# Kernel optimization log

Measured on AMD Instinct MI355X. Metric: run time of the kernel, lower is better.

The kernel has to match this reference:

```python
import jax, jax.numpy as jnp
import numpy as np

N = 100000
E = 3200000
HID = 256
C = 10
T = 12
D = 8
HEADS = 4
LH = HID // 2  # LSTM hidden = hidden_dim // 2


def setup_inputs() -> dict:
    key = jax.random.key(0)
    ks = jax.random.split(key, 16)
    rn = lambda k, shp, s=0.05: jax.random.normal(k, shp, dtype=jnp.float32) * s
    return {
        "embeddings": jax.random.normal(ks[0], (N, HID), dtype=jnp.float32),
        "predictions": jax.random.normal(ks[1], (N, C), dtype=jnp.float32),
        "temporal_features": jax.random.normal(ks[2], (N, T, D), dtype=jnp.float32),
        "edge_index": jax.random.randint(ks[3], (2, E), 0, N),
        "cW1": rn(ks[4], (HID // 2, HID)), "cb1": jnp.zeros((HID // 2,), jnp.float32),
        "cW2": rn(ks[5], (1, HID // 2)), "cb2": jnp.zeros((1,), jnp.float32),
        "w_ih0": rn(ks[6], (4 * LH, C)), "w_hh0": rn(ks[7], (4 * LH, LH)),
        "b_ih0": jnp.zeros((4 * LH,), jnp.float32), "b_hh0": jnp.zeros((4 * LH,), jnp.float32),
        "w_ih1": rn(ks[8], (4 * LH, LH)), "w_hh1": rn(ks[9], (4 * LH, LH)),
        "b_ih1": jnp.zeros((4 * LH,), jnp.float32), "b_hh1": jnp.zeros((4 * LH,), jnp.float32),
        "gW": rn(ks[10], (C, HEADS * C)), "ga_src": rn(ks[11], (HEADS, C)),
        "ga_dst": rn(ks[12], (HEADS, C)), "gb": jnp.zeros((C,), jnp.float32),
    }


def _lstm_layer(x, w_ih, w_hh, b_ih, b_hh):
    # x: [N, T, I]; PyTorch gate order i, f, g, o
    n = x.shape[0]
    h_dim = w_hh.shape[1]
    def step(carry, xt):
        h, c = carry
        g = xt @ w_ih.T + h @ w_hh.T + b_ih + b_hh  # [N, 4H]
        i, f, gg, o = jnp.split(g, 4, axis=-1)
        c = jax.nn.sigmoid(f) * c + jax.nn.sigmoid(i) * jnp.tanh(gg)
        h = jax.nn.sigmoid(o) * jnp.tanh(c)
        return (h, c), h
    init = (jnp.zeros((n, h_dim), x.dtype), jnp.zeros((n, h_dim), x.dtype))
    _, hs = jax.lax.scan(step, init, jnp.swapaxes(x, 0, 1))  # [T, N, H]
    return jnp.swapaxes(hs, 0, 1)


def _gat(probs, src, dst, gW, ga_src, ga_dst, gb, n):
    x = (probs @ gW).reshape(n, HEADS, C)  # [N, H, C]
    a_s = (x * ga_src).sum(-1)  # [N, H]
    a_d = (x * ga_dst).sum(-1)
    e = jax.nn.leaky_relu(a_s[src] + a_d[dst], 0.2)  # [E, H]
    m = jax.ops.segment_max(e, dst, num_segments=n)
    ex = jnp.exp(e - m[dst])
    s = jax.ops.segment_sum(ex, dst, num_segments=n)
    alpha = ex / (s[dst] + 1e-16)  # edge softmax per destination
    out = jax.ops.segment_sum(alpha[:, :, None] * x[src], dst, num_segments=n)
    return out.mean(axis=1) + gb  # concat=False -> head mean, plus bias


def reference(embeddings, predictions, temporal_features, edge_index,
              cW1, cb1, cW2, cb2,
              w_ih0, w_hh0, b_ih0, b_hh0, w_ih1, w_hh1, b_ih1, b_hh1,
              gW, ga_src, ga_dst, gb):
    n = predictions.shape[0]
    probs = jax.nn.softmax(predictions, axis=-1)
    max_probs = probs.max(axis=-1)
    pseudo_labels = jnp.argmax(probs, axis=-1)

    # confidence_net (dropout inactive in eval)
    h = jax.nn.relu(embeddings @ cW1.T + cb1)
    embedding_confidence = jax.nn.sigmoid(h @ cW2.T + cb2)[:, 0]

    # temporal consistency: same prediction repeated T times through 2-layer LSTM
    t = temporal_features.shape[1]
    pred_seq = jnp.broadcast_to(predictions[:, None, :], (n, t, predictions.shape[1]))
    l1 = _lstm_layer(pred_seq, w_ih0, w_hh0, b_ih0, b_hh0)
    l2 = _lstm_layer(l1, w_ih1, w_hh1, b_ih1, b_hh1)
    temporal_variance = jnp.var(l2, axis=1, ddof=1).mean(axis=-1)  # torch.var unbiased
    temporal_confidence = 1.0 / (1.0 + temporal_variance)

    # self-loops (used by both GATConv and agreement check)
    loops = jnp.arange(n, dtype=edge_index.dtype)
    src = jnp.concatenate([edge_index[0], loops])
    dst = jnp.concatenate([edge_index[1], loops])

    gout = _gat(probs, src, dst, gW, ga_src, ga_dst, gb, n)
    num = (probs * gout).sum(-1)
    den = jnp.maximum(jnp.linalg.norm(probs, axis=-1) * jnp.linalg.norm(gout, axis=-1), 1e-8)
    graph_confidence = ((num / den) + 1.0) / 2.0

    combined = (0.4 * max_probs + 0.2 * embedding_confidence
                + 0.2 * temporal_confidence + 0.2 * graph_confidence)
    confident_mask = combined > 0.85

    # neighborhood agreement via segment-sum scatter (replaces per-edge loop)
    deg = jax.ops.segment_sum(jnp.ones_like(src, jnp.float32), src, num_segments=n)
    oh = jax.nn.one_hot(pseudo_labels, C, dtype=jnp.float32)
    nsum = jax.ops.segment_sum(oh[src], dst, num_segments=n)
    navg = nsum / (deg[:, None] + 1e-8)
    agreement = jnp.take_along_axis(navg, pseudo_labels[:, None], axis=1)[:, 0] >= 0.6
    final_mask = confident_mask & agreement

    entropy = -(probs * jnp.log(probs + 1e-8)).sum(-1)
    uncertainty = entropy / np.log(C).astype(np.float32)

    return (pseudo_labels, combined, final_mask, max_probs,
            embedding_confidence, temporal_confidence, graph_confidence, uncertainty)
```

## Files before the change

### kernel.cpp

```cpp
#include <hip/hip_runtime.h>
#include <hip/hip_bf16.h>


#define HIDN 256
#define NC 10
#define TSTEPS 12
#define NHEADS 4
#define LH 128

typedef __attribute__((ext_vector_type(8))) short short8;
typedef __attribute__((ext_vector_type(4))) float floatx4;

__device__ __forceinline__ unsigned short f2bf(float x) {
  unsigned u = __float_as_uint(x);
  u = u + 0x7FFFu + ((u >> 16) & 1u);
  return (unsigned short)(u >> 16);
}
__device__ __forceinline__ unsigned char f2fp8(float x) {
  return (unsigned char)(__builtin_amdgcn_cvt_pk_fp8_f32(x, 0.f, 0, false) & 0xff);
}
__device__ __forceinline__ float fexp2(float x) { return __builtin_amdgcn_exp2f(x); }
__device__ __forceinline__ float frcpf(float x) { return __builtin_amdgcn_rcpf(x); }
#define LOG2E 1.44269504f
__device__ __forceinline__ float sigf(float x) {
  return frcpf(1.0f + fexp2(-LOG2E * x));
}
__device__ __forceinline__ float sig2(float x) {
  return frcpf(1.f + fexp2(-LOG2E * x));
}
__device__ __forceinline__ float tanh2(float x) {
  return 1.f - 2.f * frcpf(1.f + fexp2((2.f * LOG2E) * x));
}
__device__ __forceinline__ floatx4 mfma16(short8 a, short8 b, floatx4 c) {
  return __builtin_amdgcn_mfma_f32_16x16x32_bf16(a, b, c, 0, 0, 0);
}
__device__ __forceinline__ floatx4 mfma8(long a, long b, floatx4 c) {
  return __builtin_amdgcn_mfma_f32_16x16x32_fp8_fp8(a, b, c, 0, 0, 0);
}

__device__ __forceinline__ void probs_body(
    int bb, float* sgW, float* sgas, float* sgad,
    const float* __restrict__ pred, const float* __restrict__ gW,
    const float* __restrict__ gas, const float* __restrict__ gad,
    float* __restrict__ out, float* __restrict__ wp12,
    float* __restrict__ was, float* __restrict__ wad,
    int* __restrict__ wlab, float* __restrict__ wmp, int N) {
  int tid = threadIdx.x;
  for (int i = tid; i < 400; i += 256) sgW[i] = gW[i];
  if (tid < 40) { sgas[tid] = gas[tid]; sgad[tid] = gad[tid]; }
  __syncthreads();
  int node = bb * 256 + tid;
  if (node >= N) return;
  const float* pr = pred + (size_t)node * NC;
  float p[NC];
#pragma unroll
  for (int c = 0; c < NC; c++) p[c] = pr[c];
  float pm = p[0]; int arg = 0;
#pragma unroll
  for (int c = 1; c < NC; c++) if (p[c] > pm) { pm = p[c]; arg = c; }
  float s = 0.f, prb[NC];
#pragma unroll
  for (int c = 0; c < NC; c++) { prb[c] = __expf(p[c] - pm); s += prb[c]; }
  float inv = 1.f / s;
  float ent = 0.f;
#pragma unroll
  for (int c = 0; c < NC; c++) {
    prb[c] *= inv;
    ent -= prb[c] * __logf(prb[c] + 1e-8f);
  }
  float4* wp = (float4*)(wp12 + (size_t)node * 12);
  wp[0] = make_float4(prb[0], prb[1], prb[2], prb[3]);
  wp[1] = make_float4(prb[4], prb[5], prb[6], prb[7]);
  wp[2] = make_float4(prb[8], prb[9], 0.f, 0.f);
  out[node] = (float)arg;
  out[(size_t)3 * N + node] = inv;
  out[(size_t)7 * N + node] = ent * (1.f / 2.302585093f);
  wlab[node] = arg;
  wmp[node] = inv;
  float xv[40];
#pragma unroll
  for (int hc = 0; hc < 40; hc++) {
    float t = 0.f;
#pragma unroll
    for (int k = 0; k < NC; k++) t += prb[k] * sgW[k * 40 + hc];
    xv[hc] = t;
  }
#pragma unroll
  for (int h = 0; h < NHEADS; h++) {
    float as = 0.f, ad = 0.f;
#pragma unroll
    for (int c = 0; c < NC; c++) { as += xv[h * 10 + c] * sgas[h * 10 + c]; ad += xv[h * 10 + c] * sgad[h * 10 + c]; }
    was[(size_t)node * 4 + h] = as;
    wad[(size_t)node * 4 + h] = ad;
  }
}

__device__ __forceinline__ void pack_body(
    int bb, const float* __restrict__ whh0, const float* __restrict__ wih0,
    const float* __restrict__ wih1, const float* __restrict__ whh1,
    const float* __restrict__ cw1,
    unsigned char* __restrict__ PB1, unsigned char* __restrict__ PB2,
    unsigned short* __restrict__ PBc) {
  int idx = bb * 256 + threadIdx.x;
  if (idx < 81920) {
    int j = idx & 7, lane = (idx >> 3) & 63, rest = idx >> 9;
    int g = rest & 3, w = (rest >> 2) & 7, ks = rest >> 5;
    int k = ks * 32 + ((lane >> 4) << 3) + j;
    int u = w * 16 + (lane & 15), row = g * 128 + u;
    float val = 0.f;
    if (k < 128) val = whh0[row * 128 + k];
    else if (k < 138) val = wih0[row * 10 + (k - 128)];
    PB1[idx] = f2fp8(val);
  }
  if (idx < 131072) {
    int j = idx & 7, lane = (idx >> 3) & 63, rest = idx >> 9;
    int g = rest & 3, w = (rest >> 2) & 7, ks = rest >> 5;
    int k = ks * 32 + ((lane >> 4) << 3) + j;
    int u = w * 16 + (lane & 15), row = g * 128 + u;
    float val = (k < 128) ? wih1[row * 128 + k] : whh1[row * 128 + (k - 128)];
    PB2[idx] = f2fp8(val);
  }
  if (idx < 32768) {
    int j = idx & 7, lane = (idx >> 3) & 63, t2 = idx >> 9;
    int ti = t2 & 7, ks = t2 >> 3;
    int n = ti * 16 + (lane & 15);
    int k = ks * 32 + ((lane >> 4) << 3) + j;
    PBc[idx] = f2bf(cw1[n * 256 + k]);
  }
}

__device__ __forceinline__ void hist_body(
    int bb, const int* __restrict__ ei, int* __restrict__ indeg,
    int* __restrict__ outdeg, int E, int N) {
  int idx = bb * 256 + threadIdx.x;
  if (idx >= E + N) return;
  int src, dst;
  if (idx < E) { src = ei[idx]; dst = ei[E + idx]; } else { src = dst = idx - E; }
  atomicAdd(&indeg[dst], 1);
  atomicAdd(&outdeg[src], 1);
}

__global__ __launch_bounds__(256) void mega1_kernel(
    const float* __restrict__ pred, const float* __restrict__ gW,
    const float* __restrict__ gas, const float* __restrict__ gad,
    float* __restrict__ out, float* __restrict__ wp12,
    float* __restrict__ was, float* __restrict__ wad,
    int* __restrict__ wlab, float* __restrict__ wmp,
    const float* __restrict__ whh0, const float* __restrict__ wih0,
    const float* __restrict__ wih1, const float* __restrict__ whh1,
    const float* __restrict__ cw1,
    unsigned char* __restrict__ PB1, unsigned char* __restrict__ PB2,
    unsigned short* __restrict__ PBc,
    const int* __restrict__ ei, int* __restrict__ indeg, int* __restrict__ outdeg,
    int N, int E, int GP, int GK) {
  __shared__ float sgW[400], sgas[40], sgad[40];
  int b = blockIdx.x;
  if (b < GP) {
    probs_body(b, sgW, sgas, sgad, pred, gW, gas, gad, out, wp12, was, wad, wlab, wmp, N);
  } else if (b < GP + GK) {
    pack_body(b - GP, whh0, wih0, wih1, whh1, cw1, PB1, PB2, PBc);
  } else {
    hist_body(b - GP - GK, ei, indeg, outdeg, E, N);
  }
}

__device__ __forceinline__ void conf_body(
    int bb, unsigned short* astage,
    const float* __restrict__ emb, const unsigned short* __restrict__ PBc,
    const float* __restrict__ cb1, const float* __restrict__ cw2,
    const float* __restrict__ cb2, float* __restrict__ wec, int N) {
  int tid = threadIdx.x;
  int base = bb * 128;
  for (int i = tid * 4; i < 128 * 256; i += 1024) {
    int row = i >> 8, col = i & 255;
    float4 v = make_float4(0.f, 0.f, 0.f, 0.f);
    if (base + row < N) v = *(const float4*)(emb + (size_t)(base + row) * 256 + col);
    unsigned short* d = &astage[row * 264 + col];
    d[0] = f2bf(v.x); d[1] = f2bf(v.y); d[2] = f2bf(v.z); d[3] = f2bf(v.w);
  }
  __syncthreads();
  int wave = tid >> 6, lane = tid & 63, quad = lane >> 4, ln = lane & 15;
  float b1f[8], w2f[8];
#pragma unroll
  for (int t = 0; t < 8; t++) { b1f[t] = cb1[t * 16 + ln]; w2f[t] = cw2[t * 16 + ln]; }
  floatx4 acc[2][8];
#pragma unroll
  for (int mi = 0; mi < 2; mi++)
#pragma unroll
    for (int t = 0; t < 8; t++) acc[mi][t] = (floatx4){b1f[t], b1f[t], b1f[t], b1f[t]};
#pragma unroll
  for (int ks = 0; ks < 8; ks++) {
    short8 a0 = *(const short8*)&astage[(wave * 32 + ln) * 264 + ks * 32 + quad * 8];
    short8 a1 = *(const short8*)&astage[(wave * 32 + 16 + ln) * 264 + ks * 32 + quad * 8];
    const unsigned short* bp = PBc + (((size_t)(ks * 8) * 64 + lane) << 3);
#pragma unroll
    for (int t = 0; t < 8; t++) {
      short8 b = *(const short8*)(bp + (size_t)t * 512);
      acc[0][t] = mfma16(a0, b, acc[0][t]);
      acc[1][t] = mfma16(a1, b, acc[1][t]);
    }
  }
  float part[2][4];
#pragma unroll
  for (int mi = 0; mi < 2; mi++)
#pragma unroll
    for (int r = 0; r < 4; r++) {
      float t = 0.f;
#pragma unroll
      for (int ti = 0; ti < 8; ti++) t += fmaxf(acc[mi][ti][r], 0.f) * w2f[ti];
      part[mi][r] = t;
    }
#pragma unroll
  for (int off = 8; off >= 1; off >>= 1)
#pragma unroll
    for (int mi = 0; mi < 2; mi++)
#pragma unroll
      for (int r = 0; r < 4; r++) part[mi][r] += __shfl_xor(part[mi][r], off);
  if (ln == 0) {
    float b2 = cb2[0];
#pragma unroll
    for (int mi = 0; mi < 2; mi++)
#pragma unroll
      for (int r = 0; r < 4; r++) {
        int node = base + wave * 32 + mi * 16 + quad * 4 + r;
        if (node < N) wec[node] = sigf(part[mi][r] + b2);
      }
  }
}

__device__ __forceinline__ void scan_body(
    int* wsum, const int* __restrict__ indeg, int* __restrict__ rowptr,
    int* __restrict__ cursor, int N) {
  int t = threadIdx.x;
  int lane = t & 63, wv = t >> 6;
  int runbase = 0;
  for (int c0 = 0; c0 < N; c0 += 1024) {
    int i = c0 + t * 4;
    int v0 = 0, v1 = 0, v2 = 0, v3 = 0;
    if (i + 0 < N) v0 = indeg[i + 0];
    if (i + 1 < N) v1 = indeg[i + 1];
    if (i + 2 < N) v2 = indeg[i + 2];
    if (i + 3 < N) v3 = indeg[i + 3];
    int tsum = v0 + v1 + v2 + v3;
    int x = tsum;
#pragma unroll
    for (int d = 1; d < 64; d <<= 1) { int y = __shfl_up(x, d); if (lane >= d) x += y; }
    if (lane == 63) wsum[wv] = x;
    __syncthreads();
    int wo = 0;
    for (int w = 0; w < wv; w++) wo += wsum[w];
    int tot = wsum[0] + wsum[1] + wsum[2] + wsum[3];
    int excl = runbase + wo + x - tsum;
    if (i + 0 < N) { rowptr[i + 0] = excl; cursor[i + 0] = excl; }
    if (i + 1 < N) { rowptr[i + 1] = excl + v0; cursor[i + 1] = excl + v0; }
    if (i + 2 < N) { rowptr[i + 2] = excl + v0 + v1; cursor[i + 2] = excl + v0 + v1; }
    if (i + 3 < N) { rowptr[i + 3] = excl + v0 + v1 + v2; cursor[i + 3] = excl + v0 + v1 + v2; }
    runbase += tot;
    __syncthreads();
  }
  if (t == 0) rowptr[N] = runbase;
}

__global__ __launch_bounds__(256) void mega2_kernel(
    const float* __restrict__ emb, const unsigned short* __restrict__ PBc,
    const float* __restrict__ cb1, const float* __restrict__ cw2,
    const float* __restrict__ cb2, float* __restrict__ wec,
    const int* __restrict__ indeg, int* __restrict__ rowptr,
    int* __restrict__ cursor, int N, int GC) {
  __shared__ __align__(16) unsigned short astage[128 * 264];
  int b = blockIdx.x;
  if (b < GC) {
    conf_body(b, astage, emb, PBc, cb1, cw2, cb2, wec, N);
  } else {
    scan_body((int*)astage, indeg, rowptr, cursor, N);
  }
}

__global__ void scatter_kernel(const int* __restrict__ ei, int* __restrict__ cursor,
                               int* __restrict__ csr, int E, int N) {
  int idx = blockIdx.x * 256 + threadIdx.x;
  if (idx >= E + N) return;
  int src, dst;
  if (idx < E) { src = ei[idx]; dst = ei[E + idx]; } else { src = dst = idx - E; }
  int pos = atomicAdd(&cursor[dst], 1);
  csr[pos] = src;
}

__global__ __launch_bounds__(256) void gather_kernel(
    const int* __restrict__ rowptr, const int* __restrict__ csr,
    const float* __restrict__ was, const float* __restrict__ wad,
    const float* __restrict__ wp12, const int* __restrict__ wlab,
    const int* __restrict__ outdeg, const float* __restrict__ gW,
    const float* __restrict__ gb, float* __restrict__ wgc,
    float* __restrict__ wag, int N) {
  __shared__ float sgW[400];
  int tid = threadIdx.x;
  for (int i = tid; i < 400; i += 256) sgW[i] = gW[i];
  __syncthreads();
  int vgid = blockIdx.x * 256 + tid;
  int node = vgid >> 4, sub = vgid & 15, h = sub & 3, par = sub >> 2;
  if (node >= N) return;
  int beg = rowptr[node], end = rowptr[node + 1];
  float ad = wad[(size_t)node * 4 + h];
  int mylab = wlab[node];
  float ssum = 0.f, cnt = 0.f;
  float z[10];
#pragma unroll
  for (int c = 0; c < 10; c++) z[c] = 0.f;
  for (int e = beg + par; e < end; e += 4) {
    int s = csr[e];
    float v = was[(size_t)s * 4 + h] + ad;
    float lr = v >= 0.f ? v : 0.2f * v;
    float ex = fexp2(LOG2E * lr);
    ssum += ex;
    const float4* pp = (const float4*)(wp12 + (size_t)s * 12);
    float4 p0 = pp[0], p1 = pp[1], p2 = pp[2];
    z[0] += ex * p0.x; z[1] += ex * p0.y; z[2] += ex * p0.z; z[3] += ex * p0.w;
    z[4] += ex * p1.x; z[5] += ex * p1.y; z[6] += ex * p1.z; z[7] += ex * p1.w;
    z[8] += ex * p2.x; z[9] += ex * p2.y;
    cnt += (wlab[s] == mylab) ? 1.f : 0.f;
  }
  ssum += __shfl_xor(ssum, 4); ssum += __shfl_xor(ssum, 8);
  cnt  += __shfl_xor(cnt, 4);  cnt  += __shfl_xor(cnt, 8);
#pragma unroll
  for (int c = 0; c < 10; c++) { z[c] += __shfl_xor(z[c], 4); z[c] += __shfl_xor(z[c], 8); }
  float inv = 1.f / (ssum + 1e-16f);
  float gpart[10];
#pragma unroll
  for (int c = 0; c < 10; c++) {
    float t = 0.f;
#pragma unroll
    for (int k = 0; k < 10; k++) t += z[k] * sgW[k * 40 + h * 10 + c];
    gpart[c] = t * inv;
  }
#pragma unroll
  for (int c = 0; c < 10; c++) {
    gpart[c] += __shfl_xor(gpart[c], 1);
    gpart[c] += __shfl_xor(gpart[c], 2);
  }
  if (sub == 0) {
    float num = 0.f, np2 = 0.f, ng2 = 0.f;
    const float* pn = wp12 + (size_t)node * 12;
#pragma unroll
    for (int c = 0; c < 10; c++) {
      float g = gpart[c] * 0.25f + gb[c];
      float p = pn[c];
      num += p * g;
      np2 += p * p;
      ng2 += g * g;
    }
    float den = fmaxf(sqrtf(np2) * sqrtf(ng2), 1e-8f);
    wgc[node] = (num / den + 1.f) * 0.5f;
    float dgv = (float)outdeg[node];
    wag[node] = cnt / (dgv + 1e-8f);
  }
}

#define HB2 4352

__global__ __launch_bounds__(512, 2) void lstm_kernel(
    const float* __restrict__ pred, const unsigned char* __restrict__ PB1,
    const unsigned char* __restrict__ PB2,
    const float* __restrict__ bih0, const float* __restrict__ bhh0,
    const float* __restrict__ bih1, const float* __restrict__ bhh1,
    const float* __restrict__ wmp, const float* __restrict__ wec,
    const float* __restrict__ wgc, const float* __restrict__ wag,
    float* __restrict__ out, int N) {
  __shared__ __align__(16) unsigned char hb[4 * HB2];
  __shared__ __align__(16) unsigned char xbuf[32 * 40];
  __shared__ float varsum[32];
  int tid = threadIdx.x;
  int base = blockIdx.x * 32;
  for (int i = tid * 4; i < HB2; i += 2048) *(int*)&hb[3 * HB2 + i] = 0;
  for (int i = tid; i < 32 * 40; i += 512) {
    int nd = i / 40, o = i - nd * 40;
    float v = 0.f;
    if (o < 10 && base + nd < N) v = pred[(size_t)(base + nd) * NC + o];
    xbuf[i] = f2fp8(v);
  }
  if (tid < 32) varsum[tid] = 0.f;
  int wave = tid >> 6, lane = tid & 63, quad = lane >> 4, ln = lane & 15;
  float b0f[4], b1f[4];
#pragma unroll
  for (int g = 0; g < 4; g++) {
    int row = g * 128 + wave * 16 + ln;
    b0f[g] = bih0[row] + bhh0[row];
    b1f[g] = bih1[row] + bhh1[row];
  }
  long w1r[5][4], w2r[8][4];
#pragma unroll
  for (int ks = 0; ks < 5; ks++)
#pragma unroll
    for (int g = 0; g < 4; g++)
      w1r[ks][g] = *(const long*)(PB1 + (size_t)(((ks * 8 + wave) * 4 + g) * 64 + lane) * 8);
#pragma unroll
  for (int ks = 0; ks < 8; ks++)
#pragma unroll
    for (int g = 0; g < 4; g++)
      w2r[ks][g] = *(const long*)(PB2 + (size_t)(((ks * 8 + wave) * 4 + g) * 64 + lane) * 8);
  float c1[8], c2[8], s1[8], s2[8];
#pragma unroll
  for (int i = 0; i < 8; i++) { c1[i] = 0.f; c2[i] = 0.f; s1[i] = 0.f; s2[i] = 0.f; }
  const int hq = quad * 8;
  const int ucol = wave * 16 + ln;
  int arow[2], wrow[2];
#pragma unroll
  for (int mt = 0; mt < 2; mt++) {
    arow[mt] = (mt * 16 + ln) * 136 + hq;
    wrow[mt] = (mt * 16 + quad * 4) * 136 + ucol;
  }
  __syncthreads();
  long xa[2];
  xa[0] = *(const long*)&xbuf[ln * 40 + hq];
  xa[1] = *(const long*)&xbuf[(16 + ln) * 40 + hq];

  {
    floatx4 acc[2][4];
#pragma unroll
    for (int mt = 0; mt < 2; mt++)
#pragma unroll
      for (int g = 0; g < 4; g++) acc[mt][g] = (floatx4){b0f[g], b0f[g], b0f[g], b0f[g]};
#pragma unroll
    for (int g = 0; g < 4; g++)
#pragma unroll
      for (int mt = 0; mt < 2; mt++) acc[mt][g] = mfma8(xa[mt], w1r[4][g], acc[mt][g]);
#pragma unroll
    for (int mt = 0; mt < 2; mt++)
#pragma unroll
      for (int r = 0; r < 4; r++) {
        int ci = mt * 4 + r;
        float ig = sig2(acc[mt][0][r]);
        float gg = tanh2(acc[mt][2][r]);
        float og = sig2(acc[mt][3][r]);
        float c = ig * gg;
        c1[ci] = c;
        hb[0 + wrow[mt] + r * 136] = f2fp8(og * tanh2(c));
      }
  }

#define LSTM_SEG(O1R, O1W, O2R, O2W, lastseg)                                    \
  {                                                                              \
    __syncthreads();                                                             \
    floatx4 acc[2][4];                                                           \
    _Pragma("unroll") for (int mt = 0; mt < 2; mt++)                             \
        _Pragma("unroll") for (int g = 0; g < 4; g++)                            \
            acc[mt][g] = (floatx4){b1f[g], b1f[g], b1f[g], b1f[g]};              \
    _Pragma("unroll") for (int ks = 0; ks < 8; ks++) {                           \
      long a_[2];                                                                \
      if (ks < 4) {                                                              \
        _Pragma("unroll") for (int mt = 0; mt < 2; mt++)                         \
            a_[mt] = *(const long*)&hb[(O1R) + arow[mt] + ks * 32];              \
      } else {                                                                   \
        _Pragma("unroll") for (int mt = 0; mt < 2; mt++)                         \
            a_[mt] = *(const long*)&hb[(O2R) + arow[mt] + (ks - 4) * 32];        \
      }                                                                          \
      _Pragma("unroll") for (int g = 0; g < 4; g++)                              \
          _Pragma("unroll") for (int mt = 0; mt < 2; mt++)                       \
              acc[mt][g] = mfma8(a_[mt], w2r[ks][g], acc[mt][g]);                \
    }                                                                            \
    _Pragma("unroll") for (int mt = 0; mt < 2; mt++)                             \
        _Pragma("unroll") for (int r = 0; r < 4; r++) {                          \
      int ci = mt * 4 + r;                                                       \
      float ig = sig2(acc[mt][0][r]);                                            \
      float fg = sig2(acc[mt][1][r]);                                            \
      float gg = tanh2(acc[mt][2][r]);                                           \
      float og = sig2(acc[mt][3][r]);                                            \
      float c = fg * c2[ci] + ig * gg;                                           \
      c2[ci] = c;                                                                \
      float h = og * tanh2(c);                                                   \
      s1[ci] += h;                                                               \
      s2[ci] += h * h;                                                           \
      hb[(O2W) + wrow[mt] + r * 136] = f2fp8(h);                                 \
    }                                                                            \
    if (!(lastseg)) {                                                            \
      _Pragma("unroll") for (int mt = 0; mt < 2; mt++)                           \
          _Pragma("unroll") for (int g = 0; g < 4; g++)                          \
              acc[mt][g] = (floatx4){b0f[g], b0f[g], b0f[g], b0f[g]};            \
      _Pragma("unroll") for (int ks = 0; ks < 5; ks++) {                         \
        long a_[2];                                                              \
        if (ks < 4) {                                                            \
          _Pragma("unroll") for (int mt = 0; mt < 2; mt++)                       \
              a_[mt] = *(const long*)&hb[(O1R) + arow[mt] + ks * 32];            \
        } else {                                                                 \
          a_[0] = xa[0]; a_[1] = xa[1];                                          \
        }                                                                        \
        _Pragma("unroll") for (int g = 0; g < 4; g++)                            \
            _Pragma("unroll") for (int mt = 0; mt < 2; mt++)                     \
                acc[mt][g] = mfma8(a_[mt], w1r[ks][g], acc[mt][g]);              \
      }                                                                          \
      _Pragma("unroll") for (int mt = 0; mt < 2; mt++)                           \
          _Pragma("unroll") for (int r = 0; r < 4; r++) {                        \
        int ci = mt * 4 + r;                                                     \
        float ig = sig2(acc[mt][0][r]);                                          \
        float fg = sig2(acc[mt][1][r]);                                          \
        float gg = tanh2(acc[mt][2][r]);                                         \
        float og = sig2(acc[mt][3][r]);                                          \
        float c = fg * c1[ci] + ig * gg;                                         \
        c1[ci] = c;                                                              \
        hb[(O1W) + wrow[mt] + r * 136] = f2fp8(og * tanh2(c));                   \
      }                                                                          \
    }                                                                            \
  }

  for (int tt = 0; tt < TSTEPS / 2; tt++) {
    LSTM_SEG(0, HB2, 3 * HB2, 2 * HB2, false);
    LSTM_SEG(HB2, 0, 2 * HB2, 3 * HB2, tt == TSTEPS / 2 - 1);
  }
#undef LSTM_SEG

#pragma unroll
  for (int mt = 0; mt < 2; mt++)
#pragma unroll
    for (int r = 0; r < 4; r++) {
      int ci = mt * 4 + r;
      float m = s1[ci] * (1.f / 12.f);
      float var = (s2[ci] - 12.f * m * m) * (1.f / 11.f);
      atomicAdd(&varsum[mt * 16 + quad * 4 + r], var);
    }
  __syncthreads();
  if (tid < 32 && base + tid < N) {
    int node = base + tid;
    float tc = 1.f / (1.f + varsum[tid] * (1.f / 128.f));
    float mp = wmp[node], ec = wec[node], gc = wgc[node];
    float comb = 0.4f * mp + 0.2f * ec + 0.2f * tc + 0.2f * gc;
    bool mask = (comb > 0.85f) && (wag[node] >= 0.6f);
    out[(size_t)1 * N + node] = comb;
    out[(size_t)2 * N + node] = mask ? 1.f : 0.f;
    out[(size_t)4 * N + node] = ec;
    out[(size_t)5 * N + node] = tc;
    out[(size_t)6 * N + node] = gc;
  }
}

extern "C" void kernel_launch(void* const* d_in, const int* in_sizes, int n_in,
                              void* d_out, int out_size, void* d_ws, size_t ws_size,
                              hipStream_t stream) {
  const float* emb  = (const float*)d_in[0];
  const float* pred = (const float*)d_in[1];
  const int*   ei   = (const int*)d_in[3];
  const float* cw1  = (const float*)d_in[4];
  const float* cb1  = (const float*)d_in[5];
  const float* cw2  = (const float*)d_in[6];
  const float* cb2  = (const float*)d_in[7];
  const float* wih0 = (const float*)d_in[8];
  const float* whh0 = (const float*)d_in[9];
  const float* bih0 = (const float*)d_in[10];
  const float* bhh0 = (const float*)d_in[11];
  const float* wih1 = (const float*)d_in[12];
  const float* whh1 = (const float*)d_in[13];
  const float* bih1 = (const float*)d_in[14];
  const float* bhh1 = (const float*)d_in[15];
  const float* gW   = (const float*)d_in[16];
  const float* gas  = (const float*)d_in[17];
  const float* gad  = (const float*)d_in[18];
  const float* gb   = (const float*)d_in[19];

  const int N = in_sizes[0] / HIDN;
  const int E = in_sizes[3] / 2;
  float* out = (float*)d_out;
  float* ws = (float*)d_ws;
  const size_t sN = (size_t)N;

  float* wp12   = ws;
  float* was    = ws + 12 * sN;
  float* wad    = ws + 16 * sN;
  int*   wlab   = (int*)(ws + 20 * sN);
  float* wmp    = ws + 21 * sN;
  float* wec    = ws + 22 * sN;
  float* wgc    = ws + 24 * sN;
  float* wag    = ws + 25 * sN;
  int* indeg    = (int*)(ws + 26 * sN);
  int* outdeg   = (int*)(ws + 27 * sN);
  int* rowptr   = (int*)(ws + 28 * sN);
  int* cursor   = (int*)(ws + 29 * sN) + 64;
  int* csr      = (int*)(ws + 30 * sN) + 128;
  float* pbase  = ws + 31 * sN + 128 + E;
  unsigned char* PB1 = (unsigned char*)pbase;
  unsigned char* PB2 = (unsigned char*)(pbase + 20480);
  unsigned short* PBc = (unsigned short*)(pbase + 53248);

  hipMemsetAsync(indeg, 0, 2 * sN * sizeof(int), stream);

  int GP = (N + 255) / 256, GK = 512, GH = (E + N + 255) / 256;
  mega1_kernel<<<GP + GK + GH, 256, 0, stream>>>(
      pred, gW, gas, gad, out, wp12, was, wad, wlab, wmp,
      whh0, wih0, wih1, whh1, cw1, PB1, PB2, PBc,
      ei, indeg, outdeg, N, E, GP, GK);

  int GC = (N + 127) / 128;
  mega2_kernel<<<GC + 1, 256, 0, stream>>>(
      emb, PBc, cb1, cw2, cb2, wec, indeg, rowptr, cursor, N, GC);

  int ne = E + N;
  scatter_kernel<<<(ne + 255) / 256, 256, 0, stream>>>(ei, cursor, csr, E, N);

  gather_kernel<<<(16 * N + 255) / 256, 256, 0, stream>>>(
      rowptr, csr, was, wad, wp12, wlab, outdeg, gW, gb, wgc, wag, N);

  lstm_kernel<<<(N + 31) / 32, 512, 0, stream>>>(
      pred, PB1, PB2, bih0, bhh0, bih1, bhh1, wmp, wec, wgc, wag, out, N);
}
```

Baseline: 1.583 ms.

## Record per-edge rank during histogram to build CSR without scatter atomics

The in-degree histogram now keeps the value returned by its atomicAdd as each edge's rank within its destination row. The scatter step then writes csr[rowptr[dst]+rank] directly instead of doing a second round of atomics on a cursor array, and the scan no longer has to write that cursor. The fused mega1 kernel is also split back into separate probs, pack and rankhist launches. This trades atomic contention in the scatter for an extra E+N int write and read of the rank array, plus extra launch overhead and the loss of overlap between the previously fused stages.

```diff
diff --git a/kernel.cpp b/kernel.cpp
--- a/kernel.cpp
+++ b/kernel.cpp
@@ -38,18 +38,18 @@
   return __builtin_amdgcn_mfma_f32_16x16x32_fp8_fp8(a, b, c, 0, 0, 0);
 }
 
-__device__ __forceinline__ void probs_body(
-    int bb, float* sgW, float* sgas, float* sgad,
+__global__ __launch_bounds__(256) void probs_kernel(
     const float* __restrict__ pred, const float* __restrict__ gW,
     const float* __restrict__ gas, const float* __restrict__ gad,
     float* __restrict__ out, float* __restrict__ wp12,
     float* __restrict__ was, float* __restrict__ wad,
     int* __restrict__ wlab, float* __restrict__ wmp, int N) {
+  __shared__ float sgW[400], sgas[40], sgad[40];
   int tid = threadIdx.x;
   for (int i = tid; i < 400; i += 256) sgW[i] = gW[i];
   if (tid < 40) { sgas[tid] = gas[tid]; sgad[tid] = gad[tid]; }
   __syncthreads();
-  int node = bb * 256 + tid;
+  int node = blockIdx.x * 256 + tid;
   if (node >= N) return;
   const float* pr = pred + (size_t)node * NC;
   float p[NC];
@@ -95,13 +95,13 @@
   }
 }
 
-__device__ __forceinline__ void pack_body(
-    int bb, const float* __restrict__ whh0, const float* __restrict__ wih0,
+__global__ __launch_bounds__(256) void pack_kernel(
+    const float* __restrict__ whh0, const float* __restrict__ wih0,
     const float* __restrict__ wih1, const float* __restrict__ whh1,
     const float* __restrict__ cw1,
     unsigned char* __restrict__ PB1, unsigned char* __restrict__ PB2,
     unsigned short* __restrict__ PBc) {
-  int idx = bb * 256 + threadIdx.x;
+  int idx = blockIdx.x * 256 + threadIdx.x;
   if (idx < 81920) {
     int j = idx & 7, lane = (idx >> 3) & 63, rest = idx >> 9;
     int g = rest & 3, w = (rest >> 2) & 7, ks = rest >> 5;
@@ -129,39 +129,16 @@
   }
 }
 
-__device__ __forceinline__ void hist_body(
-    int bb, const int* __restrict__ ei, int* __restrict__ indeg,
-    int* __restrict__ outdeg, int E, int N) {
-  int idx = bb * 256 + threadIdx.x;
+__global__ void rankhist_kernel(const int* __restrict__ ei, int* __restrict__ indeg,
+                                int* __restrict__ outdeg, int* __restrict__ erank,
+                                int E, int N) {
+  int idx = blockIdx.x * 256 + threadIdx.x;
   if (idx >= E + N) return;
   int src, dst;
   if (idx < E) { src = ei[idx]; dst = ei[E + idx]; } else { src = dst = idx - E; }
-  atomicAdd(&indeg[dst], 1);
+  int r = atomicAdd(&indeg[dst], 1);
   atomicAdd(&outdeg[src], 1);
-}
-
-__global__ __launch_bounds__(256) void mega1_kernel(
-    const float* __restrict__ pred, const float* __restrict__ gW,
-    const float* __restrict__ gas, const float* __restrict__ gad,
-    float* __restrict__ out, float* __restrict__ wp12,
-    float* __restrict__ was, float* __restrict__ wad,
-    int* __restrict__ wlab, float* __restrict__ wmp,
-    const float* __restrict__ whh0, const float* __restrict__ wih0,
-    const float* __restrict__ wih1, const float* __restrict__ whh1,
-    const float* __restrict__ cw1,
-    unsigned char* __restrict__ PB1, unsigned char* __restrict__ PB2,
-    unsigned short* __restrict__ PBc,
-    const int* __restrict__ ei, int* __restrict__ indeg, int* __restrict__ outdeg,
-    int N, int E, int GP, int GK) {
-  __shared__ float sgW[400], sgas[40], sgad[40];
-  int b = blockIdx.x;
-  if (b < GP) {
-    probs_body(b, sgW, sgas, sgad, pred, gW, gas, gad, out, wp12, was, wad, wlab, wmp, N);
-  } else if (b < GP + GK) {
-    pack_body(b - GP, whh0, wih0, wih1, whh1, cw1, PB1, PB2, PBc);
-  } else {
-    hist_body(b - GP - GK, ei, indeg, outdeg, E, N);
-  }
+  erank[idx] = r;
 }
 
 __device__ __forceinline__ void conf_body(
@@ -229,8 +206,7 @@
 }
 
 __device__ __forceinline__ void scan_body(
-    int* wsum, const int* __restrict__ indeg, int* __restrict__ rowptr,
-    int* __restrict__ cursor, int N) {
+    int* wsum, const int* __restrict__ indeg, int* __restrict__ rowptr, int N) {
   int t = threadIdx.x;
   int lane = t & 63, wv = t >> 6;
   int runbase = 0;
@@ -251,10 +227,10 @@
     for (int w = 0; w < wv; w++) wo += wsum[w];
     int tot = wsum[0] + wsum[1] + wsum[2] + wsum[3];
     int excl = runbase + wo + x - tsum;
-    if (i + 0 < N) { rowptr[i + 0] = excl; cursor[i + 0] = excl; }
-    if (i + 1 < N) { rowptr[i + 1] = excl + v0; cursor[i + 1] = excl + v0; }
-    if (i + 2 < N) { rowptr[i + 2] = excl + v0 + v1; cursor[i + 2] = excl + v0 + v1; }
-    if (i + 3 < N) { rowptr[i + 3] = excl + v0 + v1 + v2; cursor[i + 3] = excl + v0 + v1 + v2; }
+    if (i + 0 < N) rowptr[i + 0] = excl;
+    if (i + 1 < N) rowptr[i + 1] = excl + v0;
+    if (i + 2 < N) rowptr[i + 2] = excl + v0 + v1;
+    if (i + 3 < N) rowptr[i + 3] = excl + v0 + v1 + v2;
     runbase += tot;
     __syncthreads();
   }
@@ -265,25 +241,25 @@
     const float* __restrict__ emb, const unsigned short* __restrict__ PBc,
     const float* __restrict__ cb1, const float* __restrict__ cw2,
     const float* __restrict__ cb2, float* __restrict__ wec,
-    const int* __restrict__ indeg, int* __restrict__ rowptr,
-    int* __restrict__ cursor, int N, int GC) {
+    const int* __restrict__ indeg, int* __restrict__ rowptr, int N, int GC) {
   __shared__ __align__(16) unsigned short astage[128 * 264];
   int b = blockIdx.x;
   if (b < GC) {
     conf_body(b, astage, emb, PBc, cb1, cw2, cb2, wec, N);
   } else {
-    scan_body((int*)astage, indeg, rowptr, cursor, N);
-  }
-}
-
-__global__ void scatter_kernel(const int* __restrict__ ei, int* __restrict__ cursor,
-                               int* __restrict__ csr, int E, int N) {
+    scan_body((int*)astage, indeg, rowptr, N);
+  }
+}
+
+__global__ void scatterrank_kernel(const int* __restrict__ ei,
+                                   const int* __restrict__ rowptr,
+                                   const int* __restrict__ erank,
+                                   int* __restrict__ csr, int E, int N) {
   int idx = blockIdx.x * 256 + threadIdx.x;
   if (idx >= E + N) return;
   int src, dst;
   if (idx < E) { src = ei[idx]; dst = ei[E + idx]; } else { src = dst = idx - E; }
-  int pos = atomicAdd(&cursor[dst], 1);
-  csr[pos] = src;
+  csr[rowptr[dst] + erank[idx]] = src;
 }
 
 __global__ __launch_bounds__(256) void gather_kernel(
@@ -560,6 +536,7 @@
   float* out = (float*)d_out;
   float* ws = (float*)d_ws;
   const size_t sN = (size_t)N;
+  const size_t sE = (size_t)E;
 
   float* wp12   = ws;
   float* was    = ws + 12 * sN;
@@ -572,27 +549,26 @@
   int* indeg    = (int*)(ws + 26 * sN);
   int* outdeg   = (int*)(ws + 27 * sN);
   int* rowptr   = (int*)(ws + 28 * sN);
-  int* cursor   = (int*)(ws + 29 * sN) + 64;
-  int* csr      = (int*)(ws + 30 * sN) + 128;
-  float* pbase  = ws + 31 * sN + 128 + E;
+  int* erank    = (int*)(ws + 29 * sN) + 64;
+  int* csr      = erank + sE + sN + 64;
+  float* pbase  = (float*)(csr + sE + sN + 64);
   unsigned char* PB1 = (unsigned char*)pbase;
   unsigned char* PB2 = (unsigned char*)(pbase + 20480);
   unsigned short* PBc = (unsigned short*)(pbase + 53248);
 
   hipMemsetAsync(indeg, 0, 2 * sN * sizeof(int), stream);
 
-  int GP = (N + 255) / 256, GK = 512, GH = (E + N + 255) / 256;
-  mega1_kernel<<<GP + GK + GH, 256, 0, stream>>>(
-      pred, gW, gas, gad, out, wp12, was, wad, wlab, wmp,
-      whh0, wih0, wih1, whh1, cw1, PB1, PB2, PBc,
-      ei, indeg, outdeg, N, E, GP, GK);
+  probs_kernel<<<(N + 255) / 256, 256, 0, stream>>>(
+      pred, gW, gas, gad, out, wp12, was, wad, wlab, wmp, N);
+  pack_kernel<<<512, 256, 0, stream>>>(whh0, wih0, wih1, whh1, cw1, PB1, PB2, PBc);
+  int ne = E + N;
+  rankhist_kernel<<<(ne + 255) / 256, 256, 0, stream>>>(ei, indeg, outdeg, erank, E, N);
 
   int GC = (N + 127) / 128;
   mega2_kernel<<<GC + 1, 256, 0, stream>>>(
-      emb, PBc, cb1, cw2, cb2, wec, indeg, rowptr, cursor, N, GC);
-
-  int ne = E + N;
-  scatter_kernel<<<(ne + 255) / 256, 256, 0, stream>>>(ei, cursor, csr, E, N);
+      emb, PBc, cb1, cw2, cb2, wec, indeg, rowptr, N, GC);
+
+  scatterrank_kernel<<<(ne + 255) / 256, 256, 0, stream>>>(ei, rowptr, erank, csr, E, N);
 
   gather_kernel<<<(16 * N + 255) / 256, 256, 0, stream>>>(
       rowptr, csr, was, wad, wp12, wlab, outdeg, gW, gb, wgc, wag, N);
```

Measured after the change: 1.412 ms. 10.8% less time.
